# Kernel optimization log

Hardware: AMD Instinct MI355X
Metric: run time of the kernel (lower is better)

Reference implementation:

```python
import jax, jax.numpy as jnp
import numpy as np
import math

P = 256   # state_dim
H = 1024  # hidden_dim
B = 8     # batch
L = 4096  # sequence length
R_MIN, R_MAX, THETA_MAX = 0.9, 0.999, math.pi


def _map_theta_to_A(thetas, G_diag, steps):
    cos_t = jnp.cos(thetas)
    tan_sq = jnp.tan(thetas) ** 2
    sqrt_term = 4.0 * jnp.sqrt(steps ** 4 / cos_t ** 2 + steps ** 5 * G_diag / cos_t ** 2)
    common = steps ** 2 * (-4.0 - 2.0 * steps * G_diag - 4.0 * tan_sq - 2.0 * steps * G_diag * tan_sq)
    denom = 2.0 * steps ** 4 * (1.0 + tan_sq)
    A_plus = (sqrt_term - common) / denom
    A_minus = (-sqrt_term - common) / denom
    return jnp.where(thetas > math.pi / 2, A_plus, A_minus)


def setup_inputs() -> dict:
    key = jax.random.key(0)
    k1, k2, k3, k4, k5, k6, k7 = jax.random.split(key, 7)
    x = jax.random.normal(k1, (B, L, H), dtype=jnp.float32)
    steps_raw = 0.5 * jax.random.normal(k2, (P,), dtype=jnp.float32)
    steps = jax.nn.sigmoid(steps_raw)
    mags = jnp.sqrt(jax.random.uniform(k3, (P,)) * (R_MAX ** 2 - R_MIN ** 2) + R_MIN ** 2)
    G_raw = (1.0 - mags ** 2) / (steps * mags ** 2)
    theta = jax.random.uniform(k4, (P,)) * THETA_MAX
    A_raw = _map_theta_to_A(theta, jax.nn.relu(G_raw), steps)
    std_b = 1.0 / math.sqrt(H)
    B_mat = jax.random.uniform(k5, (P, H, 2), minval=-std_b, maxval=std_b, dtype=jnp.float32)
    std_c = 1.0 / math.sqrt(P)
    C_mat = jax.random.uniform(k6, (H, P, 2), minval=-std_c, maxval=std_c, dtype=jnp.float32)
    D_vec = jax.random.normal(k7, (H,), dtype=jnp.float32)
    return {"input_sequence": x, "steps_raw": steps_raw, "G_raw": G_raw,
            "A_raw": A_raw, "B_mat": B_mat, "C_mat": C_mat, "D_vec": D_vec}


def _binary_operator(q_i, q_j):
    """Compose (M, F) pairs: (Mj@Mi, Mj@Fi + Fj); M flattened as [M11,M12,M21,M22] (4P)."""
    A_i, b_i = q_i
    A_j, b_j = q_j
    iA, iB, iC, iD = jnp.split(A_i, 4, axis=-1)
    jA, jB, jC, jD = jnp.split(A_j, 4, axis=-1)
    A_new = jnp.concatenate([jA * iA + jB * iC, jA * iB + jB * iD,
                             jC * iA + jD * iC, jC * iB + jD * iD], axis=-1)
    b_i1, b_i2 = jnp.split(b_i, 2, axis=-2)  # (..., P, 2) each
    new_b1 = jA[..., None] * b_i1 + jB[..., None] * b_i2
    new_b2 = jC[..., None] * b_i1 + jD[..., None] * b_i2
    return A_new, jnp.concatenate([new_b1, new_b2], axis=-2) + b_j


def _forward(x, steps_raw, G_raw, A_raw, B_mat, C_mat, D_vec):
    steps = jax.nn.sigmoid(steps_raw)          # (P,)
    G_diag = jax.nn.relu(G_raw)
    A_diag = jax.nn.relu(A_raw)

    Bu = jnp.einsum('blh,pht->blpt', x, B_mat)  # (B, L, P, 2)

    S = 1.0 + steps * G_diag                    # (P,)
    alpha = steps ** 2 * A_diag / S
    alpha = 1.99 * jnp.tanh(alpha / 1.99)
    M = jnp.concatenate([1.0 / S, -alpha / steps, steps / S, 1.0 - alpha])  # (4P,)
    M_exp = jnp.broadcast_to(M, (x.shape[0], x.shape[1], 4 * steps.shape[0]))

    step_b = steps[None, None, :, None]
    S_b = S[None, None, :, None]
    F1 = step_b * (1.0 / S_b) * Bu
    F2 = step_b ** 2 * (1.0 / S_b) * Bu
    F_mat = jnp.concatenate([F1, F2], axis=-2)  # (B, L, 2P, 2)

    _, xs = jax.lax.associative_scan(_binary_operator, (M_exp, F_mat), axis=1)
    ys = xs[..., steps.shape[0]:, :]            # (B, L, P, 2) -- the x-states

    Cy = jnp.einsum('blpt,hpt->blht', ys, C_mat)  # (B, L, H, 2)
    return Cy[..., 0] - Cy[..., 1] + x * D_vec


def reference(input_sequence, steps_raw, G_raw, A_raw, B_mat, C_mat, D_vec):
    return _forward(input_sequence, steps_raw, G_raw, A_raw, B_mat, C_mat, D_vec)
```

## Files before the change

### kernel.cpp

```cpp
#include <hip/hip_runtime.h>
#include <math.h>
#include <stdint.h>

#define PCH 256
#define HD  1024
#define BB  8
#define LL  4096
#define NN  512
#define MROWS (BB*LL)
#define NCH 64
#define TCH 64

typedef __bf16 bf16x8 __attribute__((ext_vector_type(8)));
typedef float  f32x4  __attribute__((ext_vector_type(4)));
typedef short  s16x8  __attribute__((ext_vector_type(8)));

#define OFFB_XBF   ((size_t)0)
#define OFFB_W1    (OFFB_XBF + (size_t)MROWS*HD*2)
#define OFFB_C2    (OFFB_W1  + (size_t)NN*HD*2)
#define OFFB_CST   (OFFB_C2  + (size_t)HD*NN*2)
#define OFFB_BU    (OFFB_CST + (size_t)16384)
#define OFFB_YS    (OFFB_BU  + (size_t)MROWS*NN*2)
#define OFFB_ZEND  (OFFB_YS  + (size_t)MROWS*NN*2)
#define OFFB_CARRY (OFFB_ZEND + (size_t)BB*NCH*2*NN*4)

__device__ __forceinline__ short f2bf(float f) {
    union { float f; uint32_t u; } v; v.f = f;
    uint32_t r = v.u + 0x7FFFu + ((v.u >> 16) & 1u);
    return (short)(r >> 16);
}
__device__ __forceinline__ float bf2f(unsigned short u) {
    union { uint32_t u; float f; } v; v.u = ((uint32_t)u) << 16;
    return v.f;
}

__global__ void prep_consts(const float* __restrict__ steps_raw,
                            const float* __restrict__ G_raw,
                            const float* __restrict__ A_raw,
                            float* __restrict__ cst) {
    int p = threadIdx.x;
    if (p >= PCH) return;
    float steps = 1.0f / (1.0f + expf(-steps_raw[p]));
    float G = fmaxf(G_raw[p], 0.0f);
    float A = fmaxf(A_raw[p], 0.0f);
    float S = 1.0f + steps * G;
    float alpha = steps * steps * A / S;
    alpha = 1.99f * tanhf(alpha / 1.99f);
    float m11 = 1.0f / S;
    float m12 = -alpha / steps;
    float m21 = steps / S;
    float m22 = 1.0f - alpha;
    float c1 = steps / S;
    float c2 = steps * steps / S;
    float a = 1.f, b = 0.f, c = 0.f, d = 1.f;
    for (int i = 0; i < TCH; ++i) {
        float na = m11*a + m12*c;
        float nb = m11*b + m12*d;
        float nc = m21*a + m22*c;
        float nd = m21*b + m22*d;
        a = na; b = nb; c = nc; d = nd;
    }
    cst[0*PCH+p] = m11; cst[1*PCH+p] = m12; cst[2*PCH+p] = m21; cst[3*PCH+p] = m22;
    cst[4*PCH+p] = c1;  cst[5*PCH+p] = c2;
    cst[6*PCH+p] = a;   cst[7*PCH+p] = b;   cst[8*PCH+p] = c;   cst[9*PCH+p] = d;
}

__global__ void prep_w(const float* __restrict__ B_mat,
                       const float* __restrict__ C_mat,
                       short* __restrict__ W1t,
                       short* __restrict__ C2t) {
    int idx = blockIdx.x * blockDim.x + threadIdx.x;
    if (idx >= HD * NN) return;
    {
        int n = idx >> 10;
        int h = idx & (HD - 1);
        int p = n >> 1, t = n & 1;
        W1t[idx] = f2bf(B_mat[(size_t)p * HD * 2 + (size_t)h * 2 + t]);
    }
    {
        int h = idx >> 9;
        int n = idx & (NN - 1);
        int p = n >> 1, t = n & 1;
        float sgn = (t == 0) ? 1.0f : -1.0f;
        C2t[idx] = f2bf(sgn * C_mat[(size_t)h * PCH * 2 + (size_t)p * 2 + t]);
    }
}

__global__ __launch_bounds__(256) void cvt_bf16(const float* __restrict__ in,
                                                short* __restrict__ out, int n8) {
    int i = blockIdx.x * blockDim.x + threadIdx.x;
    int stride = gridDim.x * blockDim.x;
    for (; i < n8; i += stride) {
        float4 a = ((const float4*)in)[2 * i];
        float4 b = ((const float4*)in)[2 * i + 1];
        s16x8 r;
        r[0] = f2bf(a.x); r[1] = f2bf(a.y); r[2] = f2bf(a.z); r[3] = f2bf(a.w);
        r[4] = f2bf(b.x); r[5] = f2bf(b.y); r[6] = f2bf(b.z); r[7] = f2bf(b.w);
        ((s16x8*)out)[i] = r;
    }
}

template <int K, int N, bool OUT_BF16, bool EPI>
__global__ __launch_bounds__(512, 2)
void gemm256(const short* __restrict__ A, const short* __restrict__ Bt,
             void* __restrict__ Cout, const short* __restrict__ xbf,
             const float* __restrict__ Dv) {
    __shared__ alignas(16) char smem[131072];
    constexpr int GX = N / 256;
    const int nwg = gridDim.x;
    const int cpx = nwg >> 3;
    const int bid = blockIdx.x;
    const int wg = (bid & 7) * cpx + (bid >> 3);
    const int by = wg / GX, bx = wg % GX;
    const int m0 = by * 256, n0 = bx * 256;

    const int tid = threadIdx.x;
    const int lane = tid & 63, w = tid >> 6;
    const int wm = w >> 2, wn = w & 3;
    const int g = lane >> 4, r16 = lane & 15;

    auto stage = [&](int buf, int k0) {
        #pragma unroll
        for (int s = 0; s < 4; ++s) {
            int c = tid + s * 512;
            int row = c >> 3, q = c & 7;
            int gq = q ^ (row & 7);
            const short* sa = A + (size_t)(m0 + row) * K + k0 + gq * 8;
            __builtin_amdgcn_global_load_lds(
                (const __attribute__((address_space(1))) void*)sa,
                (__attribute__((address_space(3))) void*)(smem + buf * 65536 + c * 16),
                16, 0, 0);
        }
        #pragma unroll
        for (int s = 0; s < 4; ++s) {
            int c = tid + s * 512;
            int row = c >> 3, q = c & 7;
            int gq = q ^ (row & 7);
            const short* sb = Bt + (size_t)(n0 + row) * K + k0 + gq * 8;
            __builtin_amdgcn_global_load_lds(
                (const __attribute__((address_space(1))) void*)sb,
                (__attribute__((address_space(3))) void*)(smem + buf * 65536 + 32768 + c * 16),
                16, 0, 0);
        }
    };

    int aoff[8], boff[4];
    #pragma unroll
    for (int mi = 0; mi < 8; ++mi) {
        int ra = wm * 128 + mi * 16 + r16;
        aoff[mi] = ra * 128 + ((g ^ (ra & 7)) << 4);
    }
    #pragma unroll
    for (int nj = 0; nj < 4; ++nj) {
        int rb = wn * 64 + nj * 16 + r16;
        boff[nj] = 32768 + rb * 128 + ((g ^ (rb & 7)) << 4);
    }

    f32x4 acc[8][4];
    #pragma unroll
    for (int mi = 0; mi < 8; ++mi)
        #pragma unroll
        for (int nj = 0; nj < 4; ++nj) acc[mi][nj] = (f32x4)0.0f;

    constexpr int NT = K / 64;
    stage(0, 0);
    __syncthreads();
    int cur = 0;
    #pragma unroll 1
    for (int t = 0; t < NT; ++t) {
        if (t + 1 < NT) stage(cur ^ 1, (t + 1) * 64);
        const char* base = smem + cur * 65536;
        #pragma unroll
        for (int kk = 0; kk < 2; ++kk) {
            bf16x8 af[8], bfv[4];
            #pragma unroll
            for (int mi = 0; mi < 8; ++mi)
                af[mi] = *(const bf16x8*)(base + (aoff[mi] ^ (kk << 6)));
            #pragma unroll
            for (int nj = 0; nj < 4; ++nj)
                bfv[nj] = *(const bf16x8*)(base + (boff[nj] ^ (kk << 6)));
            #pragma unroll
            for (int mi = 0; mi < 8; ++mi)
                #pragma unroll
                for (int nj = 0; nj < 4; ++nj)
                    acc[mi][nj] = __builtin_amdgcn_mfma_f32_16x16x32_bf16(
                        af[mi], bfv[nj], acc[mi][nj], 0, 0, 0);
        }
        __syncthreads();
        cur ^= 1;
    }

    const int crow0 = m0 + wm * 128 + g * 4;
    const int ccol0 = n0 + wn * 64 + r16;
    #pragma unroll
    for (int nj = 0; nj < 4; ++nj) {
        int col = ccol0 + nj * 16;
        float dv = EPI ? Dv[col] : 0.0f;
        #pragma unroll
        for (int mi = 0; mi < 8; ++mi) {
            #pragma unroll
            for (int r = 0; r < 4; ++r) {
                size_t idx = (size_t)(crow0 + mi * 16 + r) * N + col;
                float v = acc[mi][nj][r];
                if (EPI) v = fmaf(bf2f(((const unsigned short*)xbf)[idx]), dv, v);
                if (OUT_BF16) ((unsigned short*)Cout)[idx] = (unsigned short)f2bf(v);
                else          ((float*)Cout)[idx] = v;
            }
        }
    }
}

__global__ __launch_bounds__(512)
void scan_phase1(const unsigned short* __restrict__ Bu, const float* __restrict__ cst,
                 float* __restrict__ zend) {
    int bid = blockIdx.x;
    int b = bid / NCH, c = bid % NCH;
    int n = threadIdx.x;
    int p = n >> 1;
    float m11 = cst[0*PCH+p], m12 = cst[1*PCH+p], m21 = cst[2*PCH+p], m22 = cst[3*PCH+p];
    float c1 = cst[4*PCH+p], c2 = cst[5*PCH+p];
    float s1 = 0.f, s2 = 0.f;
    const unsigned short* bp = Bu + ((size_t)(b * LL + c * TCH)) * NN + n;
    #pragma unroll 4
    for (int i = 0; i < TCH; ++i) {
        float u = bf2f(bp[(size_t)i * NN]);
        float ns1 = fmaf(m11, s1, fmaf(m12, s2, c1 * u));
        float ns2 = fmaf(m21, s1, fmaf(m22, s2, c2 * u));
        s1 = ns1; s2 = ns2;
    }
    size_t base = ((size_t)(b * NCH + c) * 2) * NN + n;
    zend[base] = s1;
    zend[base + NN] = s2;
}

__global__ __launch_bounds__(512)
void scan_phase2(const float* __restrict__ zend, const float* __restrict__ cst,
                 float* __restrict__ carry) {
    int b = blockIdx.x;
    int n = threadIdx.x;
    int p = n >> 1;
    float a = cst[6*PCH+p], bm = cst[7*PCH+p], cmt = cst[8*PCH+p], d = cst[9*PCH+p];
    float cs1 = 0.f, cs2 = 0.f;
    for (int c = 0; c < NCH; ++c) {
        size_t base = ((size_t)(b * NCH + c) * 2) * NN + n;
        float z1 = zend[base], z2 = zend[base + NN];
        float ns1 = fmaf(a, cs1, fmaf(bm, cs2, z1));
        float ns2 = fmaf(cmt, cs1, fmaf(d, cs2, z2));
        carry[base] = ns1;
        carry[base + NN] = ns2;
        cs1 = ns1; cs2 = ns2;
    }
}

__global__ __launch_bounds__(512)
void scan_phase3(const unsigned short* __restrict__ Bu, const float* __restrict__ cst,
                 const float* __restrict__ carry, unsigned short* __restrict__ ys) {
    int bid = blockIdx.x;
    int b = bid / NCH, c = bid % NCH;
    int n = threadIdx.x;
    int p = n >> 1;
    float m11 = cst[0*PCH+p], m12 = cst[1*PCH+p], m21 = cst[2*PCH+p], m22 = cst[3*PCH+p];
    float c1 = cst[4*PCH+p], c2 = cst[5*PCH+p];
    float s1 = 0.f, s2 = 0.f;
    if (c > 0) {
        size_t base = ((size_t)(b * NCH + (c - 1)) * 2) * NN + n;
        s1 = carry[base];
        s2 = carry[base + NN];
    }
    const unsigned short* bp = Bu + ((size_t)(b * LL + c * TCH)) * NN + n;
    unsigned short* yp = ys + ((size_t)(b * LL + c * TCH)) * NN + n;
    #pragma unroll 4
    for (int i = 0; i < TCH; ++i) {
        float u = bf2f(bp[(size_t)i * NN]);
        float ns1 = fmaf(m11, s1, fmaf(m12, s2, c1 * u));
        float ns2 = fmaf(m21, s1, fmaf(m22, s2, c2 * u));
        s1 = ns1; s2 = ns2;
        yp[(size_t)i * NN] = (unsigned short)f2bf(s2);
    }
}

extern "C" void kernel_launch(void* const* d_in, const int* in_sizes, int n_in,
                              void* d_out, int out_size, void* d_ws, size_t ws_size,
                              hipStream_t stream) {
    const float* x         = (const float*)d_in[0];
    const float* steps_raw = (const float*)d_in[1];
    const float* G_raw     = (const float*)d_in[2];
    const float* A_raw     = (const float*)d_in[3];
    const float* B_mat     = (const float*)d_in[4];
    const float* C_mat     = (const float*)d_in[5];
    const float* D_vec     = (const float*)d_in[6];
    float* out = (float*)d_out;
    char*  ws  = (char*)d_ws;

    short*          xbf   = (short*)(ws + OFFB_XBF);
    short*          W1t   = (short*)(ws + OFFB_W1);
    short*          C2t   = (short*)(ws + OFFB_C2);
    float*          cst   = (float*)(ws + OFFB_CST);
    unsigned short* Bu    = (unsigned short*)(ws + OFFB_BU);
    unsigned short* ysbf  = (unsigned short*)(ws + OFFB_YS);
    float*          zend  = (float*)(ws + OFFB_ZEND);
    float*          carry = (float*)(ws + OFFB_CARRY);

    prep_consts<<<1, 256, 0, stream>>>(steps_raw, G_raw, A_raw, cst);
    prep_w<<<(HD * NN) / 512, 512, 0, stream>>>(B_mat, C_mat, W1t, C2t);
    cvt_bf16<<<2048, 256, 0, stream>>>(x, xbf, (MROWS * HD) / 8);

    gemm256<HD, NN, true, false><<<(NN / 256) * (MROWS / 256), 512, 0, stream>>>(
        xbf, W1t, (void*)Bu, nullptr, nullptr);

    scan_phase1<<<BB * NCH, 512, 0, stream>>>(Bu, cst, zend);
    scan_phase2<<<BB, 512, 0, stream>>>(zend, cst, carry);
    scan_phase3<<<BB * NCH, 512, 0, stream>>>(Bu, cst, carry, ysbf);

    gemm256<NN, HD, false, true><<<(HD / 256) * (MROWS / 256), 512, 0, stream>>>(
        (const short*)ysbf, C2t, (void*)out, xbf, D_vec);
}
```

Measured before the change: 198.6 us.

## Deepen GEMM pipeline to four half-K stages with explicit vmcnt waits

Splits each 64-wide K tile into two 32-wide stages held in a 4-slot LDS ring and keeps three stages of global-to-LDS loads in flight, using explicit s_waitcnt vmcnt counts and raw barriers in place of the single-prefetch double buffer with __syncthreads. The aim is to hide global load latency more fully behind the MFMA work. It also changes the LDS swizzle to match 64-byte rows and raises wave priority during the MFMA block. The extra barrier per half-tile and the hand-counted waitcnt values add sync overhead and correctness risk.

```diff
diff --git a/kernel.cpp b/kernel.cpp
--- a/kernel.cpp
+++ b/kernel.cpp
@@ -119,42 +119,42 @@
     const int wm = w >> 2, wn = w & 3;
     const int g = lane >> 4, r16 = lane & 15;
 
-    auto stage = [&](int buf, int k0) {
-        #pragma unroll
-        for (int s = 0; s < 4; ++s) {
+    auto stage = [&](int h) {
+        const int slot = h & 3;
+        const int k0 = (h >> 1) * 64 + (h & 1) * 32;
+        char* sbase = smem + slot * 32768;
+        #pragma unroll
+        for (int s = 0; s < 2; ++s) {
             int c = tid + s * 512;
-            int row = c >> 3, q = c & 7;
-            int gq = q ^ (row & 7);
+            int row = c >> 2, q = c & 3;
+            int gq = q ^ ((row >> 1) & 3);
             const short* sa = A + (size_t)(m0 + row) * K + k0 + gq * 8;
             __builtin_amdgcn_global_load_lds(
                 (const __attribute__((address_space(1))) void*)sa,
-                (__attribute__((address_space(3))) void*)(smem + buf * 65536 + c * 16),
+                (__attribute__((address_space(3))) void*)(sbase + c * 16),
                 16, 0, 0);
         }
         #pragma unroll
-        for (int s = 0; s < 4; ++s) {
+        for (int s = 0; s < 2; ++s) {
             int c = tid + s * 512;
-            int row = c >> 3, q = c & 7;
-            int gq = q ^ (row & 7);
+            int row = c >> 2, q = c & 3;
+            int gq = q ^ ((row >> 1) & 3);
             const short* sb = Bt + (size_t)(n0 + row) * K + k0 + gq * 8;
             __builtin_amdgcn_global_load_lds(
                 (const __attribute__((address_space(1))) void*)sb,
-                (__attribute__((address_space(3))) void*)(smem + buf * 65536 + 32768 + c * 16),
+                (__attribute__((address_space(3))) void*)(sbase + 16384 + c * 16),
                 16, 0, 0);
         }
     };
 
+    const int swzg = (g ^ ((r16 >> 1) & 3)) << 4;
     int aoff[8], boff[4];
     #pragma unroll
-    for (int mi = 0; mi < 8; ++mi) {
-        int ra = wm * 128 + mi * 16 + r16;
-        aoff[mi] = ra * 128 + ((g ^ (ra & 7)) << 4);
-    }
+    for (int mi = 0; mi < 8; ++mi)
+        aoff[mi] = (wm * 128 + mi * 16 + r16) * 64 + swzg;
     #pragma unroll
-    for (int nj = 0; nj < 4; ++nj) {
-        int rb = wn * 64 + nj * 16 + r16;
-        boff[nj] = 32768 + rb * 128 + ((g ^ (rb & 7)) << 4);
-    }
+    for (int nj = 0; nj < 4; ++nj)
+        boff[nj] = 16384 + (wn * 64 + nj * 16 + r16) * 64 + swzg;
 
     f32x4 acc[8][4];
     #pragma unroll
@@ -162,32 +162,42 @@
         #pragma unroll
         for (int nj = 0; nj < 4; ++nj) acc[mi][nj] = (f32x4)0.0f;
 
-    constexpr int NT = K / 64;
-    stage(0, 0);
-    __syncthreads();
-    int cur = 0;
-    #pragma unroll 1
-    for (int t = 0; t < NT; ++t) {
-        if (t + 1 < NT) stage(cur ^ 1, (t + 1) * 64);
-        const char* base = smem + cur * 65536;
-        #pragma unroll
-        for (int kk = 0; kk < 2; ++kk) {
-            bf16x8 af[8], bfv[4];
-            #pragma unroll
-            for (int mi = 0; mi < 8; ++mi)
-                af[mi] = *(const bf16x8*)(base + (aoff[mi] ^ (kk << 6)));
+    auto body = [&](int h) {
+        const char* base = smem + (h & 3) * 32768;
+        bf16x8 af[8], bfv[4];
+        #pragma unroll
+        for (int mi = 0; mi < 8; ++mi) af[mi] = *(const bf16x8*)(base + aoff[mi]);
+        #pragma unroll
+        for (int nj = 0; nj < 4; ++nj) bfv[nj] = *(const bf16x8*)(base + boff[nj]);
+        __builtin_amdgcn_s_setprio(1);
+        #pragma unroll
+        for (int mi = 0; mi < 8; ++mi)
             #pragma unroll
             for (int nj = 0; nj < 4; ++nj)
-                bfv[nj] = *(const bf16x8*)(base + (boff[nj] ^ (kk << 6)));
-            #pragma unroll
-            for (int mi = 0; mi < 8; ++mi)
-                #pragma unroll
-                for (int nj = 0; nj < 4; ++nj)
-                    acc[mi][nj] = __builtin_amdgcn_mfma_f32_16x16x32_bf16(
-                        af[mi], bfv[nj], acc[mi][nj], 0, 0, 0);
+                acc[mi][nj] = __builtin_amdgcn_mfma_f32_16x16x32_bf16(
+                    af[mi], bfv[nj], acc[mi][nj], 0, 0, 0);
+        __builtin_amdgcn_s_setprio(0);
+    };
+
+    constexpr int NH = (K / 64) * 2;
+    stage(0); stage(1); stage(2);
+    #pragma unroll 1
+    for (int h = 0; h < NH; ++h) {
+        const int rem = NH - 1 - h;
+        if (rem >= 3) {
+            stage(h + 3);
+            asm volatile("s_waitcnt vmcnt(12)" ::: "memory");
+        } else if (rem == 2) {
+            asm volatile("s_waitcnt vmcnt(8)" ::: "memory");
+        } else if (rem == 1) {
+            asm volatile("s_waitcnt vmcnt(4)" ::: "memory");
+        } else {
+            asm volatile("s_waitcnt vmcnt(0)" ::: "memory");
         }
-        __syncthreads();
-        cur ^= 1;
+        __builtin_amdgcn_s_barrier();
+        body(h);
+        asm volatile("s_waitcnt lgkmcnt(0)" ::: "memory");
+        __builtin_amdgcn_s_barrier();
     }
 
     const int crow0 = m0 + wm * 128 + g * 4;
```

After: 209.0 us. +5.2%, slower.

## Fuse fp32-to-bf16 conversion of x into GEMM and shrink tiles to 128

Applied to the files above, without the earlier changes.

Removes the separate cvt_bf16 pass and its bf16 copy of x. The first GEMM now loads fp32 x through registers, converts it to bf16 and writes it into LDS itself, and the final epilogue reads the fp32 residual x directly. Tiles go from 256x256 with 512 threads and K-step 64 to 128x128 with 256 threads and K-step 32, giving more blocks and higher occupancy. The cost is lower per-tile data reuse, more global traffic for the B operand, a register-staged A path instead of direct global-to-LDS loads, and an fp32 residual read in the epilogue that is twice the bytes of the old bf16 read.

```diff
diff --git a/kernel.cpp b/kernel.cpp
--- a/kernel.cpp
+++ b/kernel.cpp
@@ -15,8 +15,7 @@
 typedef float  f32x4  __attribute__((ext_vector_type(4)));
 typedef short  s16x8  __attribute__((ext_vector_type(8)));
 
-#define OFFB_XBF   ((size_t)0)
-#define OFFB_W1    (OFFB_XBF + (size_t)MROWS*HD*2)
+#define OFFB_W1    ((size_t)0)
 #define OFFB_C2    (OFFB_W1  + (size_t)NN*HD*2)
 #define OFFB_CST   (OFFB_C2  + (size_t)HD*NN*2)
 #define OFFB_BU    (OFFB_CST + (size_t)16384)
@@ -86,123 +85,147 @@
     }
 }
 
-__global__ __launch_bounds__(256) void cvt_bf16(const float* __restrict__ in,
-                                                short* __restrict__ out, int n8) {
-    int i = blockIdx.x * blockDim.x + threadIdx.x;
-    int stride = gridDim.x * blockDim.x;
-    for (; i < n8; i += stride) {
-        float4 a = ((const float4*)in)[2 * i];
-        float4 b = ((const float4*)in)[2 * i + 1];
-        s16x8 r;
-        r[0] = f2bf(a.x); r[1] = f2bf(a.y); r[2] = f2bf(a.z); r[3] = f2bf(a.w);
-        r[4] = f2bf(b.x); r[5] = f2bf(b.y); r[6] = f2bf(b.z); r[7] = f2bf(b.w);
-        ((s16x8*)out)[i] = r;
-    }
-}
-
-template <int K, int N, bool OUT_BF16, bool EPI>
-__global__ __launch_bounds__(512, 2)
-void gemm256(const short* __restrict__ A, const short* __restrict__ Bt,
-             void* __restrict__ Cout, const short* __restrict__ xbf,
+template <int K, int N, bool A_F32, bool OUT_BF16, bool EPI>
+__global__ __launch_bounds__(256, 3)
+void gemm128(const void* __restrict__ Aop, const short* __restrict__ Bt,
+             void* __restrict__ Cout, const float* __restrict__ xres,
              const float* __restrict__ Dv) {
-    __shared__ alignas(16) char smem[131072];
-    constexpr int GX = N / 256;
+    __shared__ alignas(16) char smem[32768];
+    constexpr int GX = N / 128;
     const int nwg = gridDim.x;
     const int cpx = nwg >> 3;
     const int bid = blockIdx.x;
     const int wg = (bid & 7) * cpx + (bid >> 3);
     const int by = wg / GX, bx = wg % GX;
-    const int m0 = by * 256, n0 = bx * 256;
+    const int m0 = by * 128, n0 = bx * 128;
 
     const int tid = threadIdx.x;
     const int lane = tid & 63, w = tid >> 6;
-    const int wm = w >> 2, wn = w & 3;
+    const int wm = w >> 1, wn = w & 1;
     const int g = lane >> 4, r16 = lane & 15;
 
-    auto stage = [&](int buf, int k0) {
-        #pragma unroll
-        for (int s = 0; s < 4; ++s) {
-            int c = tid + s * 512;
-            int row = c >> 3, q = c & 7;
-            int gq = q ^ (row & 7);
-            const short* sa = A + (size_t)(m0 + row) * K + k0 + gq * 8;
-            __builtin_amdgcn_global_load_lds(
-                (const __attribute__((address_space(1))) void*)sa,
-                (__attribute__((address_space(3))) void*)(smem + buf * 65536 + c * 16),
-                16, 0, 0);
-        }
-        #pragma unroll
-        for (int s = 0; s < 4; ++s) {
-            int c = tid + s * 512;
-            int row = c >> 3, q = c & 7;
-            int gq = q ^ (row & 7);
+    const short* Abf  = (const short*)Aop;
+    const float* Af32 = (const float*)Aop;
+
+    auto stageB = [&](int buf, int k0) {
+        #pragma unroll
+        for (int s = 0; s < 2; ++s) {
+            int c = tid + s * 256;
+            int row = c >> 2, q = c & 3;
+            int gq = q ^ ((row >> 1) & 3);
             const short* sb = Bt + (size_t)(n0 + row) * K + k0 + gq * 8;
             __builtin_amdgcn_global_load_lds(
                 (const __attribute__((address_space(1))) void*)sb,
-                (__attribute__((address_space(3))) void*)(smem + buf * 65536 + 32768 + c * 16),
+                (__attribute__((address_space(3))) void*)(smem + buf * 16384 + 8192 + c * 16),
                 16, 0, 0);
         }
     };
-
-    int aoff[8], boff[4];
+    auto stageAbf = [&](int buf, int k0) {
+        #pragma unroll
+        for (int s = 0; s < 2; ++s) {
+            int c = tid + s * 256;
+            int row = c >> 2, q = c & 3;
+            int gq = q ^ ((row >> 1) & 3);
+            const short* sa = Abf + (size_t)(m0 + row) * K + k0 + gq * 8;
+            __builtin_amdgcn_global_load_lds(
+                (const __attribute__((address_space(1))) void*)sa,
+                (__attribute__((address_space(3))) void*)(smem + buf * 16384 + c * 16),
+                16, 0, 0);
+        }
+    };
+    f32x4 av0, av1, av2, av3;
+    auto loadAf32 = [&](int k0) {
+        {
+            int c = tid;
+            int row = c >> 2, q = c & 3;
+            const f32x4* px = (const f32x4*)(Af32 + (size_t)(m0 + row) * K + k0 + q * 8);
+            av0 = px[0]; av1 = px[1];
+        }
+        {
+            int c = tid + 256;
+            int row = c >> 2, q = c & 3;
+            const f32x4* px = (const f32x4*)(Af32 + (size_t)(m0 + row) * K + k0 + q * 8);
+            av2 = px[0]; av3 = px[1];
+        }
+    };
+    auto writeAf32 = [&](int buf) {
+        {
+            int c = tid;
+            int row = c >> 2, q = c & 3;
+            int gq = q ^ ((row >> 1) & 3);
+            s16x8 r;
+            #pragma unroll
+            for (int j = 0; j < 4; ++j) { r[j] = f2bf(av0[j]); r[4 + j] = f2bf(av1[j]); }
+            *(s16x8*)(smem + buf * 16384 + row * 64 + gq * 16) = r;
+        }
+        {
+            int c = tid + 256;
+            int row = c >> 2, q = c & 3;
+            int gq = q ^ ((row >> 1) & 3);
+            s16x8 r;
+            #pragma unroll
+            for (int j = 0; j < 4; ++j) { r[j] = f2bf(av2[j]); r[4 + j] = f2bf(av3[j]); }
+            *(s16x8*)(smem + buf * 16384 + row * 64 + gq * 16) = r;
+        }
+    };
+
+    const int swzg = (g ^ ((r16 >> 1) & 3)) << 4;
+    int aoff[4], boff[4];
     #pragma unroll
-    for (int mi = 0; mi < 8; ++mi) {
-        int ra = wm * 128 + mi * 16 + r16;
-        aoff[mi] = ra * 128 + ((g ^ (ra & 7)) << 4);
-    }
+    for (int i = 0; i < 4; ++i)
+        aoff[i] = (wm * 64 + i * 16 + r16) * 64 + swzg;
     #pragma unroll
-    for (int nj = 0; nj < 4; ++nj) {
-        int rb = wn * 64 + nj * 16 + r16;
-        boff[nj] = 32768 + rb * 128 + ((g ^ (rb & 7)) << 4);
-    }
-
-    f32x4 acc[8][4];
+    for (int j = 0; j < 4; ++j)
+        boff[j] = 8192 + (wn * 64 + j * 16 + r16) * 64 + swzg;
+
+    f32x4 acc[4][4];
     #pragma unroll
-    for (int mi = 0; mi < 8; ++mi)
-        #pragma unroll
-        for (int nj = 0; nj < 4; ++nj) acc[mi][nj] = (f32x4)0.0f;
-
-    constexpr int NT = K / 64;
-    stage(0, 0);
+    for (int i = 0; i < 4; ++i)
+        #pragma unroll
+        for (int j = 0; j < 4; ++j) acc[i][j] = (f32x4)0.0f;
+
+    constexpr int NT = K / 32;
+    if (A_F32) { loadAf32(0); stageB(0, 0); writeAf32(0); }
+    else       { stageAbf(0, 0); stageB(0, 0); }
     __syncthreads();
     int cur = 0;
     #pragma unroll 1
     for (int t = 0; t < NT; ++t) {
-        if (t + 1 < NT) stage(cur ^ 1, (t + 1) * 64);
-        const char* base = smem + cur * 65536;
-        #pragma unroll
-        for (int kk = 0; kk < 2; ++kk) {
-            bf16x8 af[8], bfv[4];
+        if (t + 1 < NT) {
+            if (A_F32) loadAf32((t + 1) * 32);
+            else       stageAbf(cur ^ 1, (t + 1) * 32);
+            stageB(cur ^ 1, (t + 1) * 32);
+        }
+        const char* base = smem + cur * 16384;
+        bf16x8 af[4], bfv[4];
+        #pragma unroll
+        for (int i = 0; i < 4; ++i) af[i] = *(const bf16x8*)(base + aoff[i]);
+        #pragma unroll
+        for (int j = 0; j < 4; ++j) bfv[j] = *(const bf16x8*)(base + boff[j]);
+        #pragma unroll
+        for (int i = 0; i < 4; ++i)
             #pragma unroll
-            for (int mi = 0; mi < 8; ++mi)
-                af[mi] = *(const bf16x8*)(base + (aoff[mi] ^ (kk << 6)));
-            #pragma unroll
-            for (int nj = 0; nj < 4; ++nj)
-                bfv[nj] = *(const bf16x8*)(base + (boff[nj] ^ (kk << 6)));
-            #pragma unroll
-            for (int mi = 0; mi < 8; ++mi)
-                #pragma unroll
-                for (int nj = 0; nj < 4; ++nj)
-                    acc[mi][nj] = __builtin_amdgcn_mfma_f32_16x16x32_bf16(
-                        af[mi], bfv[nj], acc[mi][nj], 0, 0, 0);
-        }
+            for (int j = 0; j < 4; ++j)
+                acc[i][j] = __builtin_amdgcn_mfma_f32_16x16x32_bf16(
+                    af[i], bfv[j], acc[i][j], 0, 0, 0);
+        if (A_F32 && t + 1 < NT) writeAf32(cur ^ 1);
         __syncthreads();
         cur ^= 1;
     }
 
-    const int crow0 = m0 + wm * 128 + g * 4;
+    const int crow0 = m0 + wm * 64 + g * 4;
     const int ccol0 = n0 + wn * 64 + r16;
     #pragma unroll
-    for (int nj = 0; nj < 4; ++nj) {
-        int col = ccol0 + nj * 16;
+    for (int j = 0; j < 4; ++j) {
+        int col = ccol0 + j * 16;
         float dv = EPI ? Dv[col] : 0.0f;
         #pragma unroll
-        for (int mi = 0; mi < 8; ++mi) {
+        for (int i = 0; i < 4; ++i) {
             #pragma unroll
             for (int r = 0; r < 4; ++r) {
-                size_t idx = (size_t)(crow0 + mi * 16 + r) * N + col;
-                float v = acc[mi][nj][r];
-                if (EPI) v = fmaf(bf2f(((const unsigned short*)xbf)[idx]), dv, v);
+                size_t idx = (size_t)(crow0 + i * 16 + r) * N + col;
+                float v = acc[i][j][r];
+                if (EPI) v = fmaf(xres[idx], dv, v);
                 if (OUT_BF16) ((unsigned short*)Cout)[idx] = (unsigned short)f2bf(v);
                 else          ((float*)Cout)[idx] = v;
             }
@@ -292,7 +315,6 @@
     float* out = (float*)d_out;
     char*  ws  = (char*)d_ws;
 
-    short*          xbf   = (short*)(ws + OFFB_XBF);
     short*          W1t   = (short*)(ws + OFFB_W1);
     short*          C2t   = (short*)(ws + OFFB_C2);
     float*          cst   = (float*)(ws + OFFB_CST);
@@ -303,15 +325,14 @@
 
     prep_consts<<<1, 256, 0, stream>>>(steps_raw, G_raw, A_raw, cst);
     prep_w<<<(HD * NN) / 512, 512, 0, stream>>>(B_mat, C_mat, W1t, C2t);
-    cvt_bf16<<<2048, 256, 0, stream>>>(x, xbf, (MROWS * HD) / 8);
-
-    gemm256<HD, NN, true, false><<<(NN / 256) * (MROWS / 256), 512, 0, stream>>>(
-        xbf, W1t, (void*)Bu, nullptr, nullptr);
+
+    gemm128<HD, NN, true, true, false><<<(NN / 128) * (MROWS / 128), 256, 0, stream>>>(
+        (const void*)x, W1t, (void*)Bu, nullptr, nullptr);
 
     scan_phase1<<<BB * NCH, 512, 0, stream>>>(Bu, cst, zend);
     scan_phase2<<<BB, 512, 0, stream>>>(zend, cst, carry);
     scan_phase3<<<BB * NCH, 512, 0, stream>>>(Bu, cst, carry, ysbf);
 
-    gemm256<NN, HD, false, true><<<(HD / 256) * (MROWS / 256), 512, 0, stream>>>(
-        (const short*)ysbf, C2t, (void*)out, xbf, D_vec);
-}
+    gemm128<NN, HD, false, false, true><<<(HD / 128) * (MROWS / 128), 256, 0, stream>>>(
+        (const void*)ysbf, C2t, (void*)out, x, D_vec);
+}
```

Result: slower. 207.2 us (median of 4 runs) (+4.3%).
